# Kernel optimization log

Measured on AMD Instinct MI355X. Metric: run time of the kernel, lower is better.

The kernel has to match this reference:

```python
import jax, jax.numpy as jnp
import numpy as np

B, DIM, MID, H, W = 4, 256, 128, 128, 128
EPS = 1e-5


def _conv(x, w, pad):
    # x: [B,C,H,W], w: [O,I,k,k]
    return jax.lax.conv_general_dilated(
        x, w, window_strides=(1, 1), padding=[(pad, pad), (pad, pad)],
        dimension_numbers=('NCHW', 'OIHW', 'NCHW'))


def _bn(x, g, b, m, v):
    inv = jax.lax.rsqrt(v + EPS)
    scale = (g * inv)[None, :, None, None]
    shift = (b - m * g * inv)[None, :, None, None]
    return x * scale + shift


def _convbnrelu(x, w, g, b, m, v):
    return jax.nn.relu(_bn(_conv(x, w, 1), g, b, m, v))


# CornerNet directional pools: sequential max-accumulation scans.
def top_pool(x):     # max over y' >= y  -> reversed cummax along H
    return jax.lax.cummax(x, axis=2, reverse=True)

def bottom_pool(x):  # max over y' <= y
    return jax.lax.cummax(x, axis=2)

def left_pool(x):    # max over x' >= x
    return jax.lax.cummax(x, axis=3, reverse=True)

def right_pool(x):   # max over x' <= x
    return jax.lax.cummax(x, axis=3)


def setup_inputs() -> dict:
    key = jax.random.key(0)
    ks = jax.random.split(key, 32)
    it = iter(ks)

    def w(shape, scale=0.05):
        return jax.random.normal(next(it), shape, jnp.float32) * scale

    def bn_params(c):
        return (jnp.ones((c,), jnp.float32) + 0.1 * jax.random.normal(next(it), (c,), jnp.float32),
                0.1 * jax.random.normal(next(it), (c,), jnp.float32),
                0.1 * jax.random.normal(next(it), (c,), jnp.float32),
                jax.random.uniform(next(it), (c,), jnp.float32) + 0.5)

    inp = {'x': jax.random.normal(next(it), (B, DIM, H, W), jnp.float32)}

    inp['p1_w'] = w((MID, DIM, 3, 3))
    inp['p1_g'], inp['p1_b'], inp['p1_m'], inp['p1_v'] = bn_params(MID)
    inp['p2_w'] = w((MID, DIM, 3, 3))
    inp['p2_g'], inp['p2_b'], inp['p2_m'], inp['p2_v'] = bn_params(MID)
    inp['p_w'] = w((DIM, MID, 3, 3))
    inp['p_g'], inp['p_b'], inp['p_m'], inp['p_v'] = bn_params(DIM)
    inp['c1_w'] = w((DIM, DIM, 1, 1))
    inp['c1_g'], inp['c1_b'], inp['c1_m'], inp['c1_v'] = bn_params(DIM)
    inp['c2_w'] = w((DIM, DIM, 3, 3))
    inp['c2_g'], inp['c2_b'], inp['c2_m'], inp['c2_v'] = bn_params(DIM)
    return inp


def reference(x,
              p1_w, p1_g, p1_b, p1_m, p1_v,
              p2_w, p2_g, p2_b, p2_m, p2_v,
              p_w, p_g, p_b, p_m, p_v,
              c1_w, c1_g, c1_b, c1_m, c1_v,
              c2_w, c2_g, c2_b, c2_m, c2_v):
    # branch 1: conv-bn-relu -> top pool -> bottom pool
    pool1 = bottom_pool(top_pool(_convbnrelu(x, p1_w, p1_g, p1_b, p1_m, p1_v)))
    # branch 2: conv-bn-relu -> left pool -> right pool
    pool2 = right_pool(left_pool(_convbnrelu(x, p2_w, p2_g, p2_b, p2_m, p2_v)))
    # merge branch
    p_bn1 = _bn(_conv(pool1 + pool2, p_w, 1), p_g, p_b, p_m, p_v)
    # skip branch: 1x1 conv + bn
    bn1 = _bn(_conv(x, c1_w, 0), c1_g, c1_b, c1_m, c1_v)
    # residual add + relu, then final conv-bn-relu
    return _convbnrelu(jax.nn.relu(p_bn1 + bn1), c2_w, c2_g, c2_b, c2_m, c2_v)
```

## Files before the change

kernel.cpp:

```cpp
#include <hip/hip_runtime.h>
#include <hip/hip_bf16.h>
#include <math.h>


constexpr int NB   = 4;
constexpr int CDIM = 256;
constexpr int CMID = 128;
constexpr int HS   = 128;
constexpr int WS   = 128;
constexpr float EPS = 1e-5f;

typedef __bf16 bf16x8 __attribute__((ext_vector_type(8)));
typedef float  f32x4  __attribute__((ext_vector_type(4)));

#define AS1 __attribute__((address_space(1)))
#define AS3 __attribute__((address_space(3)))

__device__ __forceinline__ void load16_lds(const void* gsrc, void* ldst) {
    __builtin_amdgcn_global_load_lds((const AS1 unsigned int*)gsrc,
                                     (AS3 unsigned int*)ldst, 16, 0, 0);
}

__global__ __launch_bounds__(512) void k_xprep(const float* __restrict__ xin,
                                               __hip_bfloat16* __restrict__ Xc)
{
    const int y = blockIdx.x;
    const int b = blockIdx.y;
    const int t = threadIdx.x;
    __shared__ __hip_bfloat16 lds[128 * 264];
#pragma unroll
    for (int k = 0; k < 16; ++k) {
        int idx = t + k * 512;
        int ci = idx >> 5, x4 = idx & 31;
        f32x4 v = *(const f32x4*)(xin + (((size_t)b * CDIM + ci) * HS + y) * WS + x4 * 4);
#pragma unroll
        for (int j = 0; j < 4; ++j)
            lds[(x4 * 4 + j) * 264 + ci] = __float2bfloat16(v[j]);
    }
    __syncthreads();
#pragma unroll
    for (int k = 0; k < 8; ++k) {
        int i = t + k * 512;
        int x = i >> 5, c8 = i & 31;
        bf16x8 vv = *(const bf16x8*)(lds + x * 264 + c8 * 8);
        *(bf16x8*)(Xc + ((size_t)(b * 128 + y) * 128 + x) * 256 + c8 * 8) = vv;
    }
}

__global__ __launch_bounds__(256) void k_wprep_all(
    const float* __restrict__ p1w, const float* __restrict__ p2w,
    const float* __restrict__ c2w, const float* __restrict__ c1w,
    __hip_bfloat16* __restrict__ Aw1, __hip_bfloat16* __restrict__ Aw2,
    __hip_bfloat16* __restrict__ Aw5, __hip_bfloat16* __restrict__ Aw4,
    f32x4* __restrict__ zdst)
{
    const int bid = blockIdx.x;
    const int t   = threadIdx.x;
    if (bid < 512) {
        const float* W; __hip_bfloat16* A; int co;
        if (bid < 128)      { W = p1w; A = Aw1; co = bid; }
        else if (bid < 256) { W = p2w; A = Aw2; co = bid - 128; }
        else                { W = c2w; A = Aw5; co = bid - 256; }
#pragma unroll
        for (int tap = 0; tap < 9; ++tap)
            A[(size_t)co * 2304 + tap * 256 + t] =
                __float2bfloat16(W[((size_t)co * CDIM + t) * 9 + tap]);
    } else if (bid < 640) {
        int base = (bid - 512) * 512 + t;
        Aw4[base]       = __float2bfloat16(c1w[base]);
        Aw4[base + 256] = __float2bfloat16(c1w[base + 256]);
    } else if (bid < 768) {
        zdst[(size_t)(bid - 640) * 256 + t] = (f32x4){0.f, 0.f, 0.f, 0.f};
    } else {
        if (t < 16) zdst[32768 + t] = (f32x4){0.f, 0.f, 0.f, 0.f};
    }
}

template<int MODE>
__global__ __launch_bounds__(256, 2) void k_conv3(
    const __hip_bfloat16* __restrict__ Xc,
    const __hip_bfloat16* __restrict__ AwA, const __hip_bfloat16* __restrict__ AwB,
    const float* __restrict__ zbuf,
    const float* __restrict__ g1, const float* __restrict__ b1,
    const float* __restrict__ m1, const float* __restrict__ v1,
    const float* __restrict__ g2, const float* __restrict__ b2,
    const float* __restrict__ m2, const float* __restrict__ v2,
    float* __restrict__ out0, unsigned* __restrict__ cmax,
    unsigned* __restrict__ rmax, int CO)
{
    const int y0     = blockIdx.x * 2;
    const int branch = blockIdx.y;
    const int b      = blockIdx.z;
    const int co0    = (MODE == 0) ? branch * 128 : 0;

    const __hip_bfloat16* Aw = (MODE == 1 && branch) ? AwB : AwA;
    const float* gg  = (MODE == 1 && branch) ? g2 : g1;
    const float* bbp = (MODE == 1 && branch) ? b2 : b1;
    const float* mmp = (MODE == 1 && branch) ? m2 : m1;
    const float* vvp = (MODE == 1 && branch) ? v2 : v1;

    __shared__ __hip_bfloat16 smem[644 * 32];
    __shared__ float s_sc[128], s_sh[128];
    __shared__ unsigned s_red[2][128];
    char* smb = (char*)smem;

    const int t    = threadIdx.x;
    const int lane = t & 63;
    const int w    = t >> 6;
    const int ml   = lane & 15;
    const int q    = lane >> 4;
    const int mbase = (w >> 1) * 64;
    const int nbase = (w & 1) * 64;

    if (t < 128) {
        int co = co0 + t;
        float iv = rsqrtf(vvp[co] + EPS);
        float sc = gg[co] * iv;
        s_sc[t] = sc;
        s_sh[t] = bbp[co] - mmp[co] * sc;
        if (MODE == 1) { s_red[0][t] = 0u; s_red[1][t] = 0u; }
    }

    f32x4 acc[2][4][4];
#pragma unroll
    for (int yy = 0; yy < 2; ++yy)
#pragma unroll
        for (int mt = 0; mt < 4; ++mt)
#pragma unroll
            for (int nt = 0; nt < 4; ++nt)
                acc[yy][mt][nt] = (f32x4){0.f, 0.f, 0.f, 0.f};

    const __hip_bfloat16* bbase = Xc + (size_t)(b * 128) * 128 * 256;

#pragma unroll 1
    for (int ky = 0; ky < 3; ++ky) {
        const int yd0 = y0 + ky - 1;
        const __hip_bfloat16* arow = Aw + (size_t)co0 * 2304 + (3 * ky) * 256;
#pragma unroll 1
        for (int cih = 0; cih < 8; ++cih) {
            const int cb = cih * 32;
#pragma unroll
            for (int p = 0; p < 11; ++p) {
                int i = t + p * 256;
                if (i < 2576) {
                    int row = i >> 2, sl = i & 3;
                    int c = sl ^ ((row >> 1) & 3);
                    const __hip_bfloat16* src;
                    if (row < 384) {
                        int j = row >> 7, col = row & 127;
                        src = arow + (size_t)col * 2304 + j * 256 + cb + c * 8;
                    } else {
                        int rbi = row - 384;
                        int yy  = rbi >= 130;
                        int xi  = rbi - 130 * yy;
                        int gy  = yd0 + yy, gx = xi - 1;
                        src = ((unsigned)gy < 128u && (unsigned)gx < 128u)
                            ? bbase + ((size_t)(gy * 128 + gx)) * 256 + cb + c * 8
                            : (const __hip_bfloat16*)((const char*)zbuf + c * 16);
                    }
                    load16_lds(src, smb + (size_t)i * 16);
                }
            }
            __syncthreads();
#pragma unroll
            for (int j = 0; j < 3; ++j) {
                bf16x8 af[4];
#pragma unroll
                for (int mt = 0; mt < 4; ++mt) {
                    const int ra = j * 128 + mbase + mt * 16 + ml;
                    const int sa = q ^ ((ra >> 1) & 3);
                    af[mt] = *(const bf16x8*)(smb + (size_t)ra * 64 + sa * 16);
                }
#pragma unroll
                for (int yy = 0; yy < 2; ++yy) {
                    bf16x8 bfv[4];
#pragma unroll
                    for (int nt = 0; nt < 4; ++nt) {
                        const int rb = 384 + yy * 130 + nbase + nt * 16 + ml + j;
                        const int sb = q ^ ((rb >> 1) & 3);
                        bfv[nt] = *(const bf16x8*)(smb + (size_t)rb * 64 + sb * 16);
                    }
#pragma unroll
                    for (int mt = 0; mt < 4; ++mt)
#pragma unroll
                        for (int nt = 0; nt < 4; ++nt)
                            acc[yy][mt][nt] = __builtin_amdgcn_mfma_f32_16x16x32_bf16(
                                af[mt], bfv[nt], acc[yy][mt][nt], 0, 0, 0);
                }
            }
            __syncthreads();
        }
    }

#pragma unroll
    for (int mt = 0; mt < 4; ++mt) {
#pragma unroll
        for (int r = 0; r < 4; ++r) {
            const int col = mbase + mt * 16 + q * 4 + r;
            const float sc = s_sc[col], sh = s_sh[col];
            const int co = co0 + col;
            unsigned rmx0 = 0u, rmx1 = 0u;
#pragma unroll
            for (int nt = 0; nt < 4; ++nt) {
                float va = fmaxf(acc[0][mt][nt][r] * sc + sh, 0.f);
                float vb = fmaxf(acc[1][mt][nt][r] * sc + sh, 0.f);
                const int x = nbase + nt * 16 + ml;
                if (MODE == 0) {
                    out0[(((size_t)b * CO + co) * HS + y0)     * WS + x] = va;
                    out0[(((size_t)b * CO + co) * HS + y0 + 1) * WS + x] = vb;
                } else if (branch == 0) {
                    atomicMax(cmax + ((size_t)(b * 128 + co)) * 128 + x,
                              __float_as_uint(fmaxf(va, vb)));
                } else {
                    rmx0 = max(rmx0, __float_as_uint(va));
                    rmx1 = max(rmx1, __float_as_uint(vb));
                }
            }
            if (MODE == 1 && branch == 1) {
                atomicMax(&s_red[0][col], rmx0);
                atomicMax(&s_red[1][col], rmx1);
            }
        }
    }
    if (MODE == 1 && branch == 1) {
        __syncthreads();
        if (t < 128) {
            atomicMax(rmax + ((size_t)(b * 128 + t)) * 128 + y0,     s_red[0][t]);
            atomicMax(rmax + ((size_t)(b * 128 + t)) * 128 + y0 + 1, s_red[1][t]);
        }
    }
}

__global__ __launch_bounds__(128) void k_uv(
    const float* __restrict__ pw, const float* __restrict__ cm,
    const float* __restrict__ rm,
    __hip_bfloat16* __restrict__ U, __hip_bfloat16* __restrict__ V)
{
    const int co   = blockIdx.x;
    const int b    = blockIdx.y;
    const int mode = blockIdx.z;
    const int p    = threadIdx.x;
    float acc0 = 0.f, acc1 = 0.f, acc2 = 0.f;
    const float* base = (mode == 0) ? cm : rm;
    for (int ci = 0; ci < CMID; ++ci) {
        const float* w9 = pw + (co * CMID + ci) * 9;
        float s0[3], s1[3], s2[3];
        if (mode == 0) {
#pragma unroll
            for (int k = 0; k < 3; ++k) {
                float a = w9[k], qq = w9[3 + k], r = w9[6 + k];
                s0[k] = qq + r; s1[k] = a + qq + r; s2[k] = a + qq;
            }
        } else {
#pragma unroll
            for (int k = 0; k < 3; ++k) {
                float a = w9[k*3 + 0], qq = w9[k*3 + 1], r = w9[k*3 + 2];
                s0[k] = qq + r; s1[k] = a + qq + r; s2[k] = a + qq;
            }
        }
        const float* v = base + (b * CMID + ci) * 128;
#pragma unroll
        for (int k = 0; k < 3; ++k) {
            int pos = p + k - 1;
            if ((unsigned)pos < 128u) {
                float vv = v[pos];
                acc0 += s0[k] * vv; acc1 += s1[k] * vv; acc2 += s2[k] * vv;
            }
        }
    }
    __hip_bfloat16* dst = (mode == 0) ? U : V;
    dst[((0 * NB + b) * CDIM + co) * 128 + p] = __float2bfloat16(acc0);
    dst[((1 * NB + b) * CDIM + co) * 128 + p] = __float2bfloat16(acc1);
    dst[((2 * NB + b) * CDIM + co) * 128 + p] = __float2bfloat16(acc2);
}

__global__ __launch_bounds__(256, 2) void k_merge_mfma(
    const __hip_bfloat16* __restrict__ Xc, const __hip_bfloat16* __restrict__ Aw4,
    const __hip_bfloat16* __restrict__ U, const __hip_bfloat16* __restrict__ V,
    const float* __restrict__ pg, const float* __restrict__ pb,
    const float* __restrict__ pm, const float* __restrict__ pv,
    const float* __restrict__ cg, const float* __restrict__ cb,
    const float* __restrict__ cmn, const float* __restrict__ cv,
    __hip_bfloat16* __restrict__ Rc)
{
    const int y = blockIdx.x;
    const int b = blockIdx.y;
    __shared__ __hip_bfloat16 smem[32768];
    __shared__ float s_psc[256], s_psh[256], s_csc[256], s_csh[256];
    __shared__ float s_v0[256], s_vm[256], s_v1[256];
    char* smb = (char*)smem;
    const int t = threadIdx.x, lane = t & 63, w = t >> 6;
    const int ml = lane & 15, q = lane >> 4;
    const int mbase = w * 64;
    const int yc = (y == 0) ? 0 : ((y == HS - 1) ? 2 : 1);

    {
        int co = t;
        float iv = rsqrtf(pv[co] + EPS);
        float psc = pg[co] * iv;
        s_psc[co] = psc;
        s_psh[co] = pb[co] - pm[co] * psc;
        float iv2 = rsqrtf(cv[co] + EPS);
        float csc = cg[co] * iv2;
        s_csc[co] = csc;
        s_csh[co] = cb[co] - cmn[co] * csc;
        const size_t vb = ((size_t)b * CDIM + co) * 128 + y;
        const size_t cstr = (size_t)NB * CDIM * 128;
        s_v0[co] = __bfloat162float(V[vb]);
        s_vm[co] = __bfloat162float(V[cstr + vb]);
        s_v1[co] = __bfloat162float(V[2 * cstr + vb]);
    }

    f32x4 acc[4][8];
#pragma unroll
    for (int mt = 0; mt < 4; ++mt)
#pragma unroll
        for (int nt = 0; nt < 8; ++nt)
            acc[mt][nt] = (f32x4){0.f, 0.f, 0.f, 0.f};

    const __hip_bfloat16* brow = Xc + (size_t)(b * 128 + y) * 128 * 256;
#pragma unroll 1
    for (int ks = 0; ks < 4; ++ks) {
#pragma unroll
        for (int p = 0; p < 12; ++p) {
            int i   = t + p * 256;
            int row = i >> 3, sl = i & 7;
            int c   = sl ^ (row & 7);
            const __hip_bfloat16* src = (row < 256)
                ? Aw4 + (size_t)row * 256 + ks * 64 + c * 8
                : brow + (size_t)(row - 256) * 256 + ks * 64 + c * 8;
            load16_lds(src, smb + (size_t)i * 16);
        }
        __syncthreads();
#pragma unroll
        for (int s = 0; s < 2; ++s) {
            bf16x8 af[4], bfv[8];
#pragma unroll
            for (int mt = 0; mt < 4; ++mt) {
                const int ra = mbase + mt * 16 + ml;
                const int coff = ((s * 4 + q) ^ (ra & 7)) * 16;
                af[mt] = *(const bf16x8*)(smb + (size_t)ra * 128 + coff);
            }
#pragma unroll
            for (int nt = 0; nt < 8; ++nt) {
                const int rb = 256 + nt * 16 + ml;
                const int coff = ((s * 4 + q) ^ (rb & 7)) * 16;
                bfv[nt] = *(const bf16x8*)(smb + (size_t)rb * 128 + coff);
            }
#pragma unroll
            for (int mt = 0; mt < 4; ++mt)
#pragma unroll
                for (int nt = 0; nt < 8; ++nt)
                    acc[mt][nt] = __builtin_amdgcn_mfma_f32_16x16x32_bf16(
                        af[mt], bfv[nt], acc[mt][nt], 0, 0, 0);
        }
        __syncthreads();
    }

    const __hip_bfloat16* Ub = U + ((size_t)(yc * NB + b) * CDIM + mbase) * 128;
#pragma unroll
    for (int k = 0; k < 16; ++k) {
        int i = lane + k * 64;
        load16_lds(Ub + (size_t)i * 8, smb + (size_t)w * 16384 + (size_t)i * 16);
    }
    __syncthreads();
    const __hip_bfloat16* ulds = smem + w * 8192;

#pragma unroll
    for (int mt = 0; mt < 4; ++mt) {
#pragma unroll
        for (int nt = 0; nt < 8; ++nt) {
            const int x = nt * 16 + ml;
            unsigned long long pk = 0;
#pragma unroll
            for (int r = 0; r < 4; ++r) {
                const int cl = mt * 16 + q * 4 + r;
                const int co = mbase + cl;
                float u  = __bfloat162float(ulds[cl * 128 + x]);
                float vt = (x == 0) ? s_v0[co] : ((x == WS - 1) ? s_v1[co] : s_vm[co]);
                float val = fmaxf((u + vt) * s_psc[co] + s_psh[co]
                                  + acc[mt][nt][r] * s_csc[co] + s_csh[co], 0.f);
                __hip_bfloat16 hb = __float2bfloat16(val);
                unsigned short bits;
                __builtin_memcpy(&bits, &hb, 2);
                pk |= (unsigned long long)bits << (16 * r);
            }
            *(unsigned long long*)((char*)Rc +
                ((size_t)((b * 128 + y) * 128 + x) * 256 + mbase + mt * 16 + q * 4) * 2) = pk;
        }
    }
}

extern "C" void kernel_launch(void* const* d_in, const int* in_sizes, int n_in,
                              void* d_out, int out_size, void* d_ws, size_t ws_size,
                              hipStream_t stream)
{
    (void)in_sizes; (void)n_in; (void)out_size; (void)ws_size;
    const float* x    = (const float*)d_in[0];
    const float* p1_w = (const float*)d_in[1];
    const float* p1_g = (const float*)d_in[2];
    const float* p1_b = (const float*)d_in[3];
    const float* p1_m = (const float*)d_in[4];
    const float* p1_v = (const float*)d_in[5];
    const float* p2_w = (const float*)d_in[6];
    const float* p2_g = (const float*)d_in[7];
    const float* p2_b = (const float*)d_in[8];
    const float* p2_m = (const float*)d_in[9];
    const float* p2_v = (const float*)d_in[10];
    const float* p_w  = (const float*)d_in[11];
    const float* p_g  = (const float*)d_in[12];
    const float* p_b  = (const float*)d_in[13];
    const float* p_m  = (const float*)d_in[14];
    const float* p_v  = (const float*)d_in[15];
    const float* c1_w = (const float*)d_in[16];
    const float* c1_g = (const float*)d_in[17];
    const float* c1_b = (const float*)d_in[18];
    const float* c1_m = (const float*)d_in[19];
    const float* c1_v = (const float*)d_in[20];
    const float* c2_w = (const float*)d_in[21];
    const float* c2_g = (const float*)d_in[22];
    const float* c2_b = (const float*)d_in[23];
    const float* c2_m = (const float*)d_in[24];
    const float* c2_v = (const float*)d_in[25];
    float* out = (float*)d_out;
    char* ws = (char*)d_ws;

    __hip_bfloat16* Xc   = (__hip_bfloat16*)ws;
    __hip_bfloat16* Rc   = (__hip_bfloat16*)(ws + 33554432);
    __hip_bfloat16* Ubuf = (__hip_bfloat16*)(ws + 67108864);
    __hip_bfloat16* Vbuf = (__hip_bfloat16*)(ws + 67895296);
    __hip_bfloat16* Aw1  = (__hip_bfloat16*)(ws + 67108864);
    __hip_bfloat16* Aw2  = (__hip_bfloat16*)(ws + 67698688);
    __hip_bfloat16* Aw5  = (__hip_bfloat16*)(ws + 68681728);
    __hip_bfloat16* Aw4  = (__hip_bfloat16*)(ws + 69861376);
    unsigned*       cmaxU = (unsigned*)(ws + 69992448);
    unsigned*       rmaxU = (unsigned*)(ws + 70254592);
    float*          zbuf  = (float*)(ws + 70516736);

    k_wprep_all<<<dim3(769), 256, 0, stream>>>(
        p1_w, p2_w, c2_w, c1_w, Aw1, Aw2, Aw5, Aw4, (f32x4*)(ws + 69992448));
    k_xprep<<<dim3(128, 4), 512, 0, stream>>>(x, Xc);

    k_conv3<1><<<dim3(64, 2, 4), 256, 0, stream>>>(
        Xc, Aw1, Aw2, zbuf,
        p1_g, p1_b, p1_m, p1_v, p2_g, p2_b, p2_m, p2_v,
        nullptr, cmaxU, rmaxU, CMID);

    k_uv<<<dim3(256, 4, 2), 128, 0, stream>>>(
        p_w, (const float*)cmaxU, (const float*)rmaxU, Ubuf, Vbuf);

    k_merge_mfma<<<dim3(128, 4), 256, 0, stream>>>(
        Xc, Aw4, Ubuf, Vbuf, p_g, p_b, p_m, p_v,
        c1_g, c1_b, c1_m, c1_v, Rc);

    k_conv3<0><<<dim3(64, 2, 4), 256, 0, stream>>>(
        Rc, Aw5, nullptr, zbuf,
        c2_g, c2_b, c2_m, c2_v, nullptr, nullptr, nullptr, nullptr,
        out, nullptr, nullptr, CDIM);
}
```

Baseline: 392.2 us.

## Double-buffer conv3 LDS staging with 4-row tiles and 512-thread blocks

Restructures the implicit-GEMM 3x3 conv kernel to compute 4 output rows per block with 8 waves, so each staged weight tile is reused across more pixels. The ky/cin loops are flattened into 24 steps with double-buffered LDS, and the next step's global-to-LDS loads are issued in slices between the MFMA groups, using setprio around the MFMAs. For the column-max branch, per-block reduction now goes through an LDS buffer before the global atomics, which cuts global atomic traffic. The cost is about 113KB of LDS, which limits residency, and the grid halves to 256 blocks.

Result: no change. 397.3 us (+1.3%).

```diff
diff --git a/kernel.cpp b/kernel.cpp
--- a/kernel.cpp
+++ b/kernel.cpp
@@ -77,7 +77,7 @@
 }
 
 template<int MODE>
-__global__ __launch_bounds__(256, 2) void k_conv3(
+__global__ __launch_bounds__(512, 2) void k_conv3(
     const __hip_bfloat16* __restrict__ Xc,
     const __hip_bfloat16* __restrict__ AwA, const __hip_bfloat16* __restrict__ AwB,
     const float* __restrict__ zbuf,
@@ -88,7 +88,7 @@
     float* __restrict__ out0, unsigned* __restrict__ cmax,
     unsigned* __restrict__ rmax, int CO)
 {
-    const int y0     = blockIdx.x * 2;
+    const int y0     = blockIdx.x * 4;
     const int branch = blockIdx.y;
     const int b      = blockIdx.z;
     const int co0    = (MODE == 0) ? branch * 128 : 0;
@@ -99,18 +99,18 @@
     const float* mmp = (MODE == 1 && branch) ? m2 : m1;
     const float* vvp = (MODE == 1 && branch) ? v2 : v1;
 
-    __shared__ __hip_bfloat16 smem[644 * 32];
+    constexpr int BUFB = 904 * 64;
+    __shared__ alignas(16) char smb[2 * BUFB];
     __shared__ float s_sc[128], s_sh[128];
-    __shared__ unsigned s_red[2][128];
-    char* smb = (char*)smem;
+    __shared__ unsigned s_red[4][128];
 
     const int t    = threadIdx.x;
     const int lane = t & 63;
     const int w    = t >> 6;
     const int ml   = lane & 15;
     const int q    = lane >> 4;
-    const int mbase = (w >> 1) * 64;
-    const int nbase = (w & 1) * 64;
+    const int yy    = w >> 1;
+    const int mbase = (w & 1) * 64;
 
     if (t < 128) {
         int co = co0 + t;
@@ -118,115 +118,133 @@
         float sc = gg[co] * iv;
         s_sc[t] = sc;
         s_sh[t] = bbp[co] - mmp[co] * sc;
-        if (MODE == 1) { s_red[0][t] = 0u; s_red[1][t] = 0u; }
-    }
-
-    f32x4 acc[2][4][4];
-#pragma unroll
-    for (int yy = 0; yy < 2; ++yy)
-#pragma unroll
-        for (int mt = 0; mt < 4; ++mt)
-#pragma unroll
-            for (int nt = 0; nt < 4; ++nt)
-                acc[yy][mt][nt] = (f32x4){0.f, 0.f, 0.f, 0.f};
+    }
+    if (MODE == 1 && branch == 1) ((unsigned*)s_red)[t] = 0u;
+
+    f32x4 acc[4][8];
+#pragma unroll
+    for (int mt = 0; mt < 4; ++mt)
+#pragma unroll
+        for (int nt = 0; nt < 8; ++nt)
+            acc[mt][nt] = (f32x4){0.f, 0.f, 0.f, 0.f};
 
     const __hip_bfloat16* bbase = Xc + (size_t)(b * 128) * 128 * 256;
 
+    auto stage_slot = [&](int p, int nky, int ncih, char* dst) {
+        int i = t + p * 512;
+        if (i < 3616) {
+            int row = i >> 2, sl = i & 3;
+            int c = sl ^ ((row >> 1) & 3);
+            const __hip_bfloat16* src;
+            if (row < 384) {
+                int jj = row >> 7, col = row & 127;
+                src = Aw + (size_t)(co0 + col) * 2304 + (3 * nky + jj) * 256
+                         + ncih * 32 + c * 8;
+            } else {
+                int rbi = row - 384;
+                int yl  = rbi / 130;
+                int xi  = rbi - 130 * yl;
+                int gy  = y0 + nky - 1 + yl, gx = xi - 1;
+                src = ((unsigned)gy < 128u && (unsigned)gx < 128u)
+                    ? bbase + ((size_t)(gy * 128 + gx)) * 256 + ncih * 32 + c * 8
+                    : (const __hip_bfloat16*)((const char*)zbuf + c * 16);
+            }
+            load16_lds(src, dst + (size_t)i * 16);
+        }
+    };
+
+#pragma unroll
+    for (int p = 0; p < 8; ++p) stage_slot(p, 0, 0, smb);
+    __syncthreads();
+
 #pragma unroll 1
-    for (int ky = 0; ky < 3; ++ky) {
-        const int yd0 = y0 + ky - 1;
-        const __hip_bfloat16* arow = Aw + (size_t)co0 * 2304 + (3 * ky) * 256;
-#pragma unroll 1
-        for (int cih = 0; cih < 8; ++cih) {
-            const int cb = cih * 32;
-#pragma unroll
-            for (int p = 0; p < 11; ++p) {
-                int i = t + p * 256;
-                if (i < 2576) {
-                    int row = i >> 2, sl = i & 3;
-                    int c = sl ^ ((row >> 1) & 3);
-                    const __hip_bfloat16* src;
-                    if (row < 384) {
-                        int j = row >> 7, col = row & 127;
-                        src = arow + (size_t)col * 2304 + j * 256 + cb + c * 8;
-                    } else {
-                        int rbi = row - 384;
-                        int yy  = rbi >= 130;
-                        int xi  = rbi - 130 * yy;
-                        int gy  = yd0 + yy, gx = xi - 1;
-                        src = ((unsigned)gy < 128u && (unsigned)gx < 128u)
-                            ? bbase + ((size_t)(gy * 128 + gx)) * 256 + cb + c * 8
-                            : (const __hip_bfloat16*)((const char*)zbuf + c * 16);
-                    }
-                    load16_lds(src, smb + (size_t)i * 16);
+    for (int step = 0; step < 24; ++step) {
+        const char* cb_ = smb + (size_t)(step & 1) * BUFB;
+        char*       nb_ = smb + (size_t)((step + 1) & 1) * BUFB;
+        const int nstep = step + 1;
+        const int nky = nstep >> 3, ncih = nstep & 7;
+        const bool last = (step == 23);
+
+#pragma unroll
+        for (int j = 0; j < 3; ++j) {
+            bf16x8 af[4], bfv[8];
+#pragma unroll
+            for (int mt = 0; mt < 4; ++mt) {
+                const int ra = j * 128 + mbase + mt * 16 + ml;
+                const int sa = q ^ ((ra >> 1) & 3);
+                af[mt] = *(const bf16x8*)(cb_ + (size_t)ra * 64 + sa * 16);
+            }
+#pragma unroll
+            for (int nt = 0; nt < 8; ++nt) {
+                const int rb = 384 + yy * 130 + nt * 16 + ml + j;
+                const int sb = q ^ ((rb >> 1) & 3);
+                bfv[nt] = *(const bf16x8*)(cb_ + (size_t)rb * 64 + sb * 16);
+            }
+            if (!last) {
+                const int pbase = j * 3;
+                const int pcnt  = (j == 2) ? 2 : 3;
+#pragma unroll
+                for (int pp = 0; pp < pcnt; ++pp)
+                    stage_slot(pbase + pp, nky, ncih, nb_);
+            }
+            __builtin_amdgcn_s_barrier();
+            __builtin_amdgcn_s_setprio(1);
+#pragma unroll
+            for (int mt = 0; mt < 4; ++mt)
+#pragma unroll
+                for (int nt = 0; nt < 8; ++nt)
+                    acc[mt][nt] = __builtin_amdgcn_mfma_f32_16x16x32_bf16(
+                        af[mt], bfv[nt], acc[mt][nt], 0, 0, 0);
+            __builtin_amdgcn_s_setprio(0);
+            __builtin_amdgcn_s_barrier();
+        }
+        __syncthreads();
+    }
+
+    if (MODE == 1 && branch == 0) {
+        unsigned* colred = (unsigned*)smb;
+#pragma unroll
+        for (int k2 = 0; k2 < 32; ++k2) colred[t + k2 * 512] = 0u;
+        __syncthreads();
+    }
+
+#pragma unroll
+    for (int mt = 0; mt < 4; ++mt) {
+#pragma unroll
+        for (int r = 0; r < 4; ++r) {
+            const int cl = mbase + mt * 16 + q * 4 + r;
+            const float sc = s_sc[cl], sh = s_sh[cl];
+            const int co = co0 + cl;
+            unsigned rmx = 0u;
+#pragma unroll
+            for (int nt = 0; nt < 8; ++nt) {
+                float va = fmaxf(acc[mt][nt][r] * sc + sh, 0.f);
+                const int x = nt * 16 + ml;
+                if (MODE == 0) {
+                    out0[(((size_t)b * CO + co) * HS + y0 + yy) * WS + x] = va;
+                } else if (branch == 0) {
+                    atomicMax(((unsigned*)smb) + cl * 128 + x, __float_as_uint(va));
+                } else {
+                    rmx = max(rmx, __float_as_uint(va));
                 }
             }
-            __syncthreads();
-#pragma unroll
-            for (int j = 0; j < 3; ++j) {
-                bf16x8 af[4];
-#pragma unroll
-                for (int mt = 0; mt < 4; ++mt) {
-                    const int ra = j * 128 + mbase + mt * 16 + ml;
-                    const int sa = q ^ ((ra >> 1) & 3);
-                    af[mt] = *(const bf16x8*)(smb + (size_t)ra * 64 + sa * 16);
-                }
-#pragma unroll
-                for (int yy = 0; yy < 2; ++yy) {
-                    bf16x8 bfv[4];
-#pragma unroll
-                    for (int nt = 0; nt < 4; ++nt) {
-                        const int rb = 384 + yy * 130 + nbase + nt * 16 + ml + j;
-                        const int sb = q ^ ((rb >> 1) & 3);
-                        bfv[nt] = *(const bf16x8*)(smb + (size_t)rb * 64 + sb * 16);
-                    }
-#pragma unroll
-                    for (int mt = 0; mt < 4; ++mt)
-#pragma unroll
-                        for (int nt = 0; nt < 4; ++nt)
-                            acc[yy][mt][nt] = __builtin_amdgcn_mfma_f32_16x16x32_bf16(
-                                af[mt], bfv[nt], acc[yy][mt][nt], 0, 0, 0);
-                }
-            }
-            __syncthreads();
-        }
-    }
-
-#pragma unroll
-    for (int mt = 0; mt < 4; ++mt) {
-#pragma unroll
-        for (int r = 0; r < 4; ++r) {
-            const int col = mbase + mt * 16 + q * 4 + r;
-            const float sc = s_sc[col], sh = s_sh[col];
-            const int co = co0 + col;
-            unsigned rmx0 = 0u, rmx1 = 0u;
-#pragma unroll
-            for (int nt = 0; nt < 4; ++nt) {
-                float va = fmaxf(acc[0][mt][nt][r] * sc + sh, 0.f);
-                float vb = fmaxf(acc[1][mt][nt][r] * sc + sh, 0.f);
-                const int x = nbase + nt * 16 + ml;
-                if (MODE == 0) {
-                    out0[(((size_t)b * CO + co) * HS + y0)     * WS + x] = va;
-                    out0[(((size_t)b * CO + co) * HS + y0 + 1) * WS + x] = vb;
-                } else if (branch == 0) {
-                    atomicMax(cmax + ((size_t)(b * 128 + co)) * 128 + x,
-                              __float_as_uint(fmaxf(va, vb)));
-                } else {
-                    rmx0 = max(rmx0, __float_as_uint(va));
-                    rmx1 = max(rmx1, __float_as_uint(vb));
-                }
-            }
-            if (MODE == 1 && branch == 1) {
-                atomicMax(&s_red[0][col], rmx0);
-                atomicMax(&s_red[1][col], rmx1);
-            }
-        }
-    }
-    if (MODE == 1 && branch == 1) {
+            if (MODE == 1 && branch == 1) atomicMax(&s_red[yy][cl], rmx);
+        }
+    }
+
+    if (MODE == 1) {
         __syncthreads();
-        if (t < 128) {
-            atomicMax(rmax + ((size_t)(b * 128 + t)) * 128 + y0,     s_red[0][t]);
-            atomicMax(rmax + ((size_t)(b * 128 + t)) * 128 + y0 + 1, s_red[1][t]);
+        if (branch == 0) {
+            unsigned* colred = (unsigned*)smb;
+#pragma unroll
+            for (int k2 = 0; k2 < 32; ++k2) {
+                int idx = t + k2 * 512;
+                atomicMax(cmax + ((size_t)(b * 128 + (idx >> 7))) * 128 + (idx & 127),
+                          colred[idx]);
+            }
+        } else {
+            atomicMax(rmax + ((size_t)(b * 128 + (t & 127))) * 128 + y0 + (t >> 7),
+                      s_red[t >> 7][t & 127]);
         }
     }
 }
@@ -441,7 +459,7 @@
         p1_w, p2_w, c2_w, c1_w, Aw1, Aw2, Aw5, Aw4, (f32x4*)(ws + 69992448));
     k_xprep<<<dim3(128, 4), 512, 0, stream>>>(x, Xc);
 
-    k_conv3<1><<<dim3(64, 2, 4), 256, 0, stream>>>(
+    k_conv3<1><<<dim3(32, 2, 4), 512, 0, stream>>>(
         Xc, Aw1, Aw2, zbuf,
         p1_g, p1_b, p1_m, p1_v, p2_g, p2_b, p2_m, p2_v,
         nullptr, cmaxU, rmaxU, CMID);
@@ -453,7 +471,7 @@
         Xc, Aw4, Ubuf, Vbuf, p_g, p_b, p_m, p_v,
         c1_g, c1_b, c1_m, c1_v, Rc);
 
-    k_conv3<0><<<dim3(64, 2, 4), 256, 0, stream>>>(
+    k_conv3<0><<<dim3(32, 2, 4), 512, 0, stream>>>(
         Rc, Aw5, nullptr, zbuf,
         c2_g, c2_b, c2_m, c2_v, nullptr, nullptr, nullptr, nullptr,
         out, nullptr, nullptr, CDIM);
```

## Merge input and weight prep kernels; remap conv blocks for XCD locality

Applied to the files above, without the earlier changes.

The x-transpose and weight-conversion kernels are merged into one 512-thread launch, with weight blocks each handling two 256-thread units. The conv kernel's block index is remapped so that blocks landing on the same XCD (round-robin by flat id) share a batch image and a contiguous range of rows. This is meant to improve L2 reuse of input halos and weights per XCD and to remove one launch. The mapping assumes 8 XCDs with round-robin dispatch, and every weight-prep block now statically allocates the large LDS array even though it does not use it.

After: 403.7 us. 2.9% more time.

```diff
diff --git a/kernel.cpp b/kernel.cpp
--- a/kernel.cpp
+++ b/kernel.cpp
@@ -21,58 +21,60 @@
                                      (AS3 unsigned int*)ldst, 16, 0, 0);
 }
 
-__global__ __launch_bounds__(512) void k_xprep(const float* __restrict__ xin,
-                                               __hip_bfloat16* __restrict__ Xc)
-{
-    const int y = blockIdx.x;
-    const int b = blockIdx.y;
-    const int t = threadIdx.x;
-    __shared__ __hip_bfloat16 lds[128 * 264];
-#pragma unroll
-    for (int k = 0; k < 16; ++k) {
-        int idx = t + k * 512;
-        int ci = idx >> 5, x4 = idx & 31;
-        f32x4 v = *(const f32x4*)(xin + (((size_t)b * CDIM + ci) * HS + y) * WS + x4 * 4);
-#pragma unroll
-        for (int j = 0; j < 4; ++j)
-            lds[(x4 * 4 + j) * 264 + ci] = __float2bfloat16(v[j]);
-    }
-    __syncthreads();
-#pragma unroll
-    for (int k = 0; k < 8; ++k) {
-        int i = t + k * 512;
-        int x = i >> 5, c8 = i & 31;
-        bf16x8 vv = *(const bf16x8*)(lds + x * 264 + c8 * 8);
-        *(bf16x8*)(Xc + ((size_t)(b * 128 + y) * 128 + x) * 256 + c8 * 8) = vv;
-    }
-}
-
-__global__ __launch_bounds__(256) void k_wprep_all(
+__global__ __launch_bounds__(512) void k_prep(
+    const float* __restrict__ xin, __hip_bfloat16* __restrict__ Xc,
     const float* __restrict__ p1w, const float* __restrict__ p2w,
     const float* __restrict__ c2w, const float* __restrict__ c1w,
     __hip_bfloat16* __restrict__ Aw1, __hip_bfloat16* __restrict__ Aw2,
     __hip_bfloat16* __restrict__ Aw5, __hip_bfloat16* __restrict__ Aw4,
     f32x4* __restrict__ zdst)
 {
+    __shared__ __hip_bfloat16 lds[128 * 264];
     const int bid = blockIdx.x;
     const int t   = threadIdx.x;
+
     if (bid < 512) {
+        const int y = bid >> 2;
+        const int b = bid & 3;
+#pragma unroll
+        for (int k = 0; k < 16; ++k) {
+            int idx = t + k * 512;
+            int ci = idx >> 5, x4 = idx & 31;
+            f32x4 v = *(const f32x4*)(xin + (((size_t)b * CDIM + ci) * HS + y) * WS + x4 * 4);
+#pragma unroll
+            for (int j = 0; j < 4; ++j)
+                lds[(x4 * 4 + j) * 264 + ci] = __float2bfloat16(v[j]);
+        }
+        __syncthreads();
+#pragma unroll
+        for (int k = 0; k < 8; ++k) {
+            int i = t + k * 512;
+            int x = i >> 5, c8 = i & 31;
+            bf16x8 vv = *(const bf16x8*)(lds + x * 264 + c8 * 8);
+            *(bf16x8*)(Xc + ((size_t)(b * 128 + y) * 128 + x) * 256 + c8 * 8) = vv;
+        }
+        return;
+    }
+
+    const int u  = (bid - 512) * 2 + (t >> 8);
+    const int tl = t & 255;
+    if (u < 512) {
         const float* W; __hip_bfloat16* A; int co;
-        if (bid < 128)      { W = p1w; A = Aw1; co = bid; }
-        else if (bid < 256) { W = p2w; A = Aw2; co = bid - 128; }
-        else                { W = c2w; A = Aw5; co = bid - 256; }
+        if (u < 128)      { W = p1w; A = Aw1; co = u; }
+        else if (u < 256) { W = p2w; A = Aw2; co = u - 128; }
+        else              { W = c2w; A = Aw5; co = u - 256; }
 #pragma unroll
         for (int tap = 0; tap < 9; ++tap)
-            A[(size_t)co * 2304 + tap * 256 + t] =
-                __float2bfloat16(W[((size_t)co * CDIM + t) * 9 + tap]);
-    } else if (bid < 640) {
-        int base = (bid - 512) * 512 + t;
+            A[(size_t)co * 2304 + tap * 256 + tl] =
+                __float2bfloat16(W[((size_t)co * CDIM + tl) * 9 + tap]);
+    } else if (u < 640) {
+        int base = (u - 512) * 512 + tl;
         Aw4[base]       = __float2bfloat16(c1w[base]);
         Aw4[base + 256] = __float2bfloat16(c1w[base + 256]);
-    } else if (bid < 768) {
-        zdst[(size_t)(bid - 640) * 256 + t] = (f32x4){0.f, 0.f, 0.f, 0.f};
-    } else {
-        if (t < 16) zdst[32768 + t] = (f32x4){0.f, 0.f, 0.f, 0.f};
+    } else if (u < 768) {
+        zdst[(size_t)(u - 640) * 256 + tl] = (f32x4){0.f, 0.f, 0.f, 0.f};
+    } else if (u == 768) {
+        if (tl < 16) zdst[32768 + tl] = (f32x4){0.f, 0.f, 0.f, 0.f};
     }
 }
 
@@ -88,9 +90,12 @@
     float* __restrict__ out0, unsigned* __restrict__ cmax,
     unsigned* __restrict__ rmax, int CO)
 {
-    const int y0     = blockIdx.x * 2;
-    const int branch = blockIdx.y;
-    const int b      = blockIdx.z;
+    const int flat   = blockIdx.x + 64 * (blockIdx.y + 2 * blockIdx.z);
+    const int xcd    = flat & 7;
+    const int g      = flat >> 3;
+    const int b      = xcd >> 1;
+    const int branch = g >> 5;
+    const int y0     = ((xcd & 1) * 32 + (g & 31)) * 2;
     const int co0    = (MODE == 0) ? branch * 128 : 0;
 
     const __hip_bfloat16* Aw = (MODE == 1 && branch) ? AwB : AwA;
@@ -437,9 +442,9 @@
     unsigned*       rmaxU = (unsigned*)(ws + 70254592);
     float*          zbuf  = (float*)(ws + 70516736);
 
-    k_wprep_all<<<dim3(769), 256, 0, stream>>>(
-        p1_w, p2_w, c2_w, c1_w, Aw1, Aw2, Aw5, Aw4, (f32x4*)(ws + 69992448));
-    k_xprep<<<dim3(128, 4), 512, 0, stream>>>(x, Xc);
+    k_prep<<<dim3(897), 512, 0, stream>>>(
+        x, Xc, p1_w, p2_w, c2_w, c1_w, Aw1, Aw2, Aw5, Aw4,
+        (f32x4*)(ws + 69992448));
 
     k_conv3<1><<<dim3(64, 2, 4), 256, 0, stream>>>(
         Xc, Aw1, Aw2, zbuf,
```
